# Kernel optimization log

Hardware: AMD Instinct MI355X
Metric: run time of the kernel (lower is better)

The kernel has to match this reference:

```python
import jax, jax.numpy as jnp
import numpy as np
import math

B, T, C, H = 2, 1024, 1024, 16
D = C // H


def setup_inputs() -> dict:
    key = jax.random.key(0)
    ks = jax.random.split(key, 7)
    scale = 1.0 / math.sqrt(C)
    q = jax.random.normal(ks[0], (B, T, C), dtype=jnp.float32)
    k = jax.random.normal(ks[1], (B, T, C), dtype=jnp.float32)
    v = jax.random.normal(ks[2], (B, T, C), dtype=jnp.float32)
    # causal mask, True = masked out (matches create_causal_mask)
    mask = jnp.triu(jnp.ones((T, T), dtype=bool), k=1)[None, None]
    Wk = jax.random.normal(ks[3], (C, C), dtype=jnp.float32) * scale
    bk = jax.random.normal(ks[4], (C,), dtype=jnp.float32) * scale
    Wc = jax.random.normal(ks[5], (C, C), dtype=jnp.float32) * scale
    bc = jax.random.normal(ks[6], (C,), dtype=jnp.float32) * scale
    return {"q": q, "k": k, "v": v, "mask": mask, "Wk": Wk, "bk": bk, "Wc": Wc, "bc": bc}


def reference(q, k, v, mask, Wk, bk, Wc, bc):
    # NOTE: original module uses self.k_attn for ALL of q, k, v (q_attn/v_attn unused).
    qB, qT, qC = q.shape
    kT = k.shape[1]
    qp = (q @ Wk.T + bk).reshape(qB, qT, H, D).transpose(0, 2, 1, 3)  # [B,H,Tq,D]
    kp = (k @ Wk.T + bk).reshape(qB, kT, H, D).transpose(0, 2, 1, 3)  # [B,H,Tk,D]
    vp = (v @ Wk.T + bk).reshape(qB, kT, H, D).transpose(0, 2, 1, 3)  # [B,H,Tk,D]
    att = jnp.einsum('bhqd,bhkd->bhqk', qp, kp) * (1.0 / math.sqrt(D))
    att = jnp.where(mask, -jnp.inf, att)
    att = jax.nn.softmax(att, axis=-1)
    y = jnp.einsum('bhqk,bhkd->bhqd', att, vp)
    y = y.transpose(0, 2, 1, 3).reshape(qB, qT, qC)
    return y @ Wc.T + bc
```

## Files before the change

### kernel.cpp

```cpp
#include <hip/hip_runtime.h>

#define T_DIM 1024
#define C_DIM 1024
#define H_DIM 16
#define D_DIM 64
#define KD    1024

typedef short  short8  __attribute__((ext_vector_type(8)));
typedef short  short4v __attribute__((ext_vector_type(4)));
typedef float  f32x4   __attribute__((ext_vector_type(4)));

__device__ __forceinline__ float bf2f(short s) {
  return __uint_as_float(((unsigned)(unsigned short)s) << 16);
}
__device__ __forceinline__ short f2bf(float f) {
  unsigned u = __float_as_uint(f);
  u += 0x7fffu + ((u >> 16) & 1u);
  return (short)(u >> 16);
}
__device__ __forceinline__ unsigned pk2(float lo, float hi) {
  return ((unsigned)(unsigned short)f2bf(lo)) | (((unsigned)(unsigned short)f2bf(hi)) << 16);
}

__device__ __forceinline__ void gl2lds16(const short* g, short* l) {
  __builtin_amdgcn_global_load_lds(
      (const __attribute__((address_space(1))) unsigned int*)(const void*)g,
      (__attribute__((address_space(3))) unsigned int*)(void*)l,
      16, 0, 0);
}

__device__ __forceinline__ short8 ldfrag(const void* p, size_t off, int isf32) {
  if (isf32) {
    const float* q = (const float*)p + off;
    f32x4 lo = *(const f32x4*)q;
    f32x4 hi = *(const f32x4*)(q + 4);
    short8 r;
#pragma unroll
    for (int j = 0; j < 4; ++j) { r[j] = f2bf(lo[j]); r[j + 4] = f2bf(hi[j]); }
    return r;
  }
  return *(const short8*)((const short*)p + off);
}
__device__ __forceinline__ float ldbias(const void* b, int i, int isf32) {
  return isf32 ? ((const float*)b)[i] : bf2f(((const short*)b)[i]);
}

__device__ __forceinline__ int detect_f32_inblock(const unsigned* w, int lane) {
  int c = 0;
#pragma unroll
  for (int i = 0; i < 4; ++i) {
    unsigned e = (w[lane * 4 + i] >> 7) & 0xffu;
    c += (e >= 110u && e <= 135u) ? 1 : 0;
  }
#pragma unroll
  for (int off = 32; off; off >>= 1) c += __shfl_xor(c, off);
  return (c < 128) ? 1 : 0;
}

#define SZE  ((size_t)2 * T_DIM * C_DIM)
#define QN   ((size_t)2097152)
#define WN   ((size_t)1048576)
#define BN   ((size_t)1024)
#define CVT_TOT (3 * QN + 2 * WN + 2 * BN)

__global__ __launch_bounds__(256) void cvt_k(const void* __restrict__ q,
                                             const void* __restrict__ k,
                                             const void* __restrict__ v,
                                             const void* __restrict__ wk,
                                             const void* __restrict__ wc,
                                             const void* __restrict__ bk,
                                             const void* __restrict__ bc,
                                             short* __restrict__ dst)
{
  const int lane = threadIdx.x & 63;
  const int f = detect_f32_inblock((const unsigned*)q, lane);

  const size_t idx = (size_t)blockIdx.x * 1024 + threadIdx.x * 4;
  if (idx >= CVT_TOT) return;
  const void* src;
  size_t loc;
  if      (idx <     QN)          { src = q;  loc = idx; }
  else if (idx < 2 * QN)          { src = k;  loc = idx - QN; }
  else if (idx < 3 * QN)          { src = v;  loc = idx - 2 * QN; }
  else if (idx < 3 * QN + WN)     { src = wk; loc = idx - 3 * QN; }
  else if (idx < 3 * QN + 2 * WN) { src = wc; loc = idx - 3 * QN - WN; }
  else if (idx < 3 * QN + 2 * WN + BN) { src = bk; loc = idx - 3 * QN - 2 * WN; }
  else                            { src = bc; loc = idx - 3 * QN - 2 * WN - BN; }

  short4v o;
  if (f) {
    f32x4 x = *(const f32x4*)((const float*)src + loc);
#pragma unroll
    for (int j = 0; j < 4; ++j) o[j] = f2bf(x[j]);
  } else {
    o = *(const short4v*)((const short*)src + loc);
  }
  *(short4v*)(dst + idx) = o;
}

__device__ __forceinline__ void stage8x8(const short* gsrc, short* S, int R0,
                                         int lane, int koff) {
  const int rw = R0 + (lane >> 3);
  const int q  = (lane & 7) ^ (rw & 7);
  gl2lds16(gsrc + (size_t)rw * KD + koff + q * 8, &S[R0 * 64]);
}
__device__ __forceinline__ short8 fragread64(const short* S, int row, int chunk) {
  const int sl = (row << 3) + (chunk ^ (row & 7));
  return *(const short8*)&S[sl << 3];
}

__global__ __launch_bounds__(256) void gemm_qkv_a(const short* __restrict__ X0,
                                                  const short* __restrict__ X1,
                                                  const short* __restrict__ X2,
                                                  const short* __restrict__ Wv,
                                                  const short* __restrict__ Bv,
                                                  short* __restrict__ outv)
{
  const int tid  = threadIdx.x;
  const int lane = tid & 63;
  const int wave = tid >> 6;
  const int col16 = lane & 15;
  const int quad  = lane >> 4;

  const int m0 = blockIdx.x * 128;
  const int c0 = blockIdx.y * 64;

  const int src = m0 >> 11;
  const short* Xv = (src == 0) ? X0 : (src == 1) ? X1 : X2;
  const int arow = m0 & 2047;
  const bool isv = (src == 2);
  short* outb = outv + (size_t)src * SZE;

  __shared__ short As[128 * 64];
  __shared__ short Bs[64 * 64];

  const short* Xg = Xv + (size_t)arow * KD;
  const short* Wg = Wv + (size_t)c0 * KD;

  f32x4 acc[2][4] = {};

  for (int k0 = 0; k0 < KD; k0 += 64) {
    if (k0) __syncthreads();
    stage8x8(Xg, As, wave * 32,      lane, k0);
    stage8x8(Xg, As, wave * 32 + 8,  lane, k0);
    stage8x8(Xg, As, wave * 32 + 16, lane, k0);
    stage8x8(Xg, As, wave * 32 + 24, lane, k0);
    stage8x8(Wg, Bs, wave * 16,      lane, k0);
    stage8x8(Wg, Bs, wave * 16 + 8,  lane, k0);
    __syncthreads();

#pragma unroll
    for (int kk = 0; kk < 2; ++kk) {
      short8 fx[2], fw[4];
#pragma unroll
      for (int i = 0; i < 2; ++i)
        fx[i] = fragread64(As, wave * 32 + i * 16 + col16, kk * 4 + quad);
#pragma unroll
      for (int j = 0; j < 4; ++j)
        fw[j] = fragread64(Bs, j * 16 + col16, kk * 4 + quad);

      if (isv) {
#pragma unroll
        for (int i = 0; i < 2; ++i)
#pragma unroll
          for (int j = 0; j < 4; ++j)
            acc[i][j] = __builtin_amdgcn_mfma_f32_16x16x32_bf16(fx[i], fw[j], acc[i][j], 0, 0, 0);
      } else {
#pragma unroll
        for (int i = 0; i < 2; ++i)
#pragma unroll
          for (int j = 0; j < 4; ++j)
            acc[i][j] = __builtin_amdgcn_mfma_f32_16x16x32_bf16(fw[j], fx[i], acc[i][j], 0, 0, 0);
      }
    }
  }

  if (isv) {
#pragma unroll
    for (int i = 0; i < 2; ++i) {
#pragma unroll
      for (int j = 0; j < 4; ++j) {
        const int c  = c0 + j * 16 + col16;
        const int t0 = arow + wave * 32 + i * 16 + quad * 4;
        const float bv = bf2f(Bv[c]);
        short4v pk;
#pragma unroll
        for (int r = 0; r < 4; ++r) pk[r] = f2bf(acc[i][j][r] + bv);
        const int bb = t0 >> 10, t = t0 & 1023, h = c >> 6, d = c & 63;
        size_t off = (size_t)((bb * H_DIM + h) * D_DIM + d) * T_DIM + t;
        *(short4v*)(outb + off) = pk;
      }
    }
  } else {
#pragma unroll
    for (int i = 0; i < 2; ++i) {
#pragma unroll
      for (int j = 0; j < 4; ++j) {
        const int m  = arow + wave * 32 + i * 16 + col16;
        const int cb = c0 + j * 16 + quad * 4;
        short4v bv4 = *(const short4v*)(Bv + cb);
        short4v pk;
#pragma unroll
        for (int r = 0; r < 4; ++r) pk[r] = f2bf(acc[i][j][r] + bf2f(bv4[r]));
        const int bb = m >> 10, t = m & 1023, h = cb >> 6, d = cb & 63;
        size_t off = ((size_t)(bb * H_DIM + h) << 16) + (size_t)t * D_DIM + d;
        *(short4v*)(outb + off) = pk;
      }
    }
  }
}

__global__ __launch_bounds__(256) void gemm_out_a(const short* __restrict__ Xb,
                                                  const short* __restrict__ Wv,
                                                  const short* __restrict__ Bv,
                                                  float* __restrict__ outv)
{
  const int tid  = threadIdx.x;
  const int lane = tid & 63;
  const int wave = tid >> 6;
  const int col16 = lane & 15;
  const int quad  = lane >> 4;
  const int wm = wave & 1;
  const int wn = wave >> 1;

  const int m0 = blockIdx.x * 64;
  const int c0 = blockIdx.y * 64;

  __shared__ short As[64 * 64];
  __shared__ short Bs[64 * 64];

  const short* Xg = Xb + (size_t)m0 * KD;
  const short* Wg = Wv + (size_t)c0 * KD;

  f32x4 acc[2][2] = {};

  for (int k0 = 0; k0 < KD; k0 += 64) {
    if (k0) __syncthreads();
    stage8x8(Xg, As, wave * 16,     lane, k0);
    stage8x8(Xg, As, wave * 16 + 8, lane, k0);
    stage8x8(Wg, Bs, wave * 16,     lane, k0);
    stage8x8(Wg, Bs, wave * 16 + 8, lane, k0);
    __syncthreads();

#pragma unroll
    for (int kk = 0; kk < 2; ++kk) {
      short8 fx[2], fw[2];
#pragma unroll
      for (int i = 0; i < 2; ++i)
        fx[i] = fragread64(As, wm * 32 + i * 16 + col16, kk * 4 + quad);
#pragma unroll
      for (int j = 0; j < 2; ++j)
        fw[j] = fragread64(Bs, wn * 32 + j * 16 + col16, kk * 4 + quad);

#pragma unroll
      for (int i = 0; i < 2; ++i)
#pragma unroll
        for (int j = 0; j < 2; ++j)
          acc[i][j] = __builtin_amdgcn_mfma_f32_16x16x32_bf16(fw[j], fx[i], acc[i][j], 0, 0, 0);
    }
  }

#pragma unroll
  for (int i = 0; i < 2; ++i) {
#pragma unroll
    for (int j = 0; j < 2; ++j) {
      const int m  = m0 + wm * 32 + i * 16 + col16;
      const int cb = c0 + wn * 32 + j * 16 + quad * 4;
      f32x4 pv;
#pragma unroll
      for (int r = 0; r < 4; ++r) pv[r] = acc[i][j][r] + bf2f(Bv[cb + r]);
      *(f32x4*)(outv + (size_t)m * C_DIM + cb) = pv;
    }
  }
}

#define LDSP 40

template<int KIND>
__global__ __launch_bounds__(256) void gemm2_k(const void* __restrict__ X0,
                                               const void* __restrict__ X1,
                                               const void* __restrict__ X2,
                                               const void* __restrict__ Wv,
                                               const void* __restrict__ Bv,
                                               void* __restrict__ outv)
{
  const int tid  = threadIdx.x;
  const int lane = tid & 63;
  const int wave = tid >> 6;
  const int col16 = lane & 15;
  const int quad  = lane >> 4;
  const int wm = wave & 1;
  const int wn = wave >> 1;

  const int f  = detect_f32_inblock((const unsigned*)Wv, lane);
  const int wf = f;
  const int xf = (KIND == 1) ? f : 0;

  const int m0 = blockIdx.x * 64;
  const int c0 = blockIdx.y * 64;

  const void* Xv = X0;
  int arow = m0;
  bool isv = false;
  short* outb = (short*)outv;
  if (KIND == 1) {
    const int src = m0 >> 11;
    Xv = (src == 0) ? X0 : (src == 1) ? X1 : X2;
    arow = m0 & 2047;
    isv = (src == 2);
    outb = (short*)outv + (size_t)src * SZE;
  }

  __shared__ short As[64 * LDSP];
  __shared__ short Bs[64 * LDSP];

  const int srow = tid >> 2;
  const int sc8  = tid & 3;

  f32x4 acc[2][2] = {};

  for (int k0 = 0; k0 < KD; k0 += 32) {
    short8 va = ldfrag(Xv, (size_t)(arow + srow) * KD + k0 + sc8 * 8, xf);
    short8 vb = ldfrag(Wv, (size_t)(c0 + srow) * KD + k0 + sc8 * 8, wf);
    if (k0) __syncthreads();
    *(short8*)&As[srow * LDSP + sc8 * 8] = va;
    *(short8*)&Bs[srow * LDSP + sc8 * 8] = vb;
    __syncthreads();

    short8 fx[2], fw[2];
#pragma unroll
    for (int i = 0; i < 2; ++i)
      fx[i] = *(const short8*)&As[(wm * 32 + i * 16 + col16) * LDSP + quad * 8];
#pragma unroll
    for (int j = 0; j < 2; ++j)
      fw[j] = *(const short8*)&Bs[(wn * 32 + j * 16 + col16) * LDSP + quad * 8];

    if (KIND == 1 && isv) {
#pragma unroll
      for (int i = 0; i < 2; ++i)
#pragma unroll
        for (int j = 0; j < 2; ++j)
          acc[i][j] = __builtin_amdgcn_mfma_f32_16x16x32_bf16(fx[i], fw[j], acc[i][j], 0, 0, 0);
    } else {
#pragma unroll
      for (int i = 0; i < 2; ++i)
#pragma unroll
        for (int j = 0; j < 2; ++j)
          acc[i][j] = __builtin_amdgcn_mfma_f32_16x16x32_bf16(fw[j], fx[i], acc[i][j], 0, 0, 0);
    }
  }

  if (KIND == 1 && isv) {
#pragma unroll
    for (int i = 0; i < 2; ++i) {
#pragma unroll
      for (int j = 0; j < 2; ++j) {
        const int c  = c0 + wn * 32 + j * 16 + col16;
        const int t0 = arow + wm * 32 + i * 16 + quad * 4;
        const float bv = ldbias(Bv, c, wf);
        short4v pk;
#pragma unroll
        for (int r = 0; r < 4; ++r) pk[r] = f2bf(acc[i][j][r] + bv);
        const int bb = t0 >> 10, t = t0 & 1023, h = c >> 6, d = c & 63;
        size_t off = (size_t)((bb * H_DIM + h) * D_DIM + d) * T_DIM + t;
        *(short4v*)(outb + off) = pk;
      }
    }
  } else {
#pragma unroll
    for (int i = 0; i < 2; ++i) {
#pragma unroll
      for (int j = 0; j < 2; ++j) {
        const int m  = arow + wm * 32 + i * 16 + col16;
        const int cb = c0 + wn * 32 + j * 16 + quad * 4;
        if (KIND == 0) {
          f32x4 pv;
#pragma unroll
          for (int r = 0; r < 4; ++r) pv[r] = acc[i][j][r] + ldbias(Bv, cb + r, wf);
          *(f32x4*)((float*)outv + (size_t)m * C_DIM + cb) = pv;
        } else {
          short4v pk;
#pragma unroll
          for (int r = 0; r < 4; ++r) pk[r] = f2bf(acc[i][j][r] + ldbias(Bv, cb + r, wf));
          const int bb = m >> 10, t = m & 1023, h = cb >> 6, d = cb & 63;
          size_t off = ((size_t)(bb * H_DIM + h) << 16) + (size_t)t * D_DIM + d;
          *(short4v*)(outb + off) = pk;
        }
      }
    }
  }
}

__global__ __launch_bounds__(256) void attn_k3(const short* __restrict__ qp,
                                               const short* __restrict__ kp,
                                               const short* __restrict__ vpt,
                                               short* __restrict__ y)
{
  const int lane = threadIdx.x & 63;
  const int wave = threadIdx.x >> 6;
  const int col  = lane & 15;
  const int quad = lane >> 4;
  const int bh = blockIdx.x;
  const int b = bh >> 4, h = bh & 15;
  const int qt = 63 - (int)blockIdx.y;
  const int q0 = qt * 16;
  const int myq = q0 + col;

  const short* qph = qp  + (size_t)bh * (T_DIM * D_DIM);
  const short* kph = kp  + (size_t)bh * (T_DIM * D_DIM);
  const short* vph = vpt + (size_t)bh * (D_DIM * T_DIM);

  const int nkt  = (q0 + 47) >> 5;
  const int base = nkt >> 2, rem = nkt & 3;
  const int cnt   = base + (wave < rem ? 1 : 0);
  const int start = wave * base + (wave < rem ? wave : rem);

  short8 bQ[2];
#pragma unroll
  for (int kk = 0; kk < 2; ++kk)
    bQ[kk] = *(const short8*)(qph + (size_t)(q0 + col) * D_DIM + kk * 32 + quad * 8);

  f32x4 O[4] = {};
  float rs = 0.0f;

  const int slA = col + ((quad & 1) * 32);
  const int slB = slA + 16;

#pragma unroll 2
  for (int kt = start; kt < start + cnt; ++kt) {
    const int kb = kt * 32;
    f32x4 st[2];
#pragma unroll
    for (int jt = 0; jt < 2; ++jt) {
      f32x4 s = {0.f, 0.f, 0.f, 0.f};
      const short* kbase = kph + (size_t)(kb + jt * 16 + col) * D_DIM + quad * 8;
      short8 aK0 = *(const short8*)(kbase);
      short8 aK1 = *(const short8*)(kbase + 32);
      __builtin_amdgcn_s_setprio(1);
      s = __builtin_amdgcn_mfma_f32_16x16x32_bf16(aK0, bQ[0], s, 0, 0, 0);
      s = __builtin_amdgcn_mfma_f32_16x16x32_bf16(aK1, bQ[1], s, 0, 0, 0);
      __builtin_amdgcn_s_setprio(0);
      st[jt] = s;
    }
#pragma unroll
    for (int jt = 0; jt < 2; ++jt) {
#pragma unroll
      for (int r = 0; r < 4; ++r) {
        const int key = kb + jt * 16 + quad * 4 + r;
        float p = __expf(st[jt][r] * 0.125f);
        p = (key > myq) ? 0.0f : p;
        st[jt][r] = p;
        rs += p;
      }
    }

    const int a0 = (int)pk2(st[0][0], st[0][1]);
    const int a1 = (int)pk2(st[0][2], st[0][3]);
    const int b0 = (int)pk2(st[1][0], st[1][1]);
    const int b1 = (int)pk2(st[1][2], st[1][3]);
    const int tA0 = __shfl(a0, slA, 64), tB0 = __shfl(b0, slA, 64);
    const int tA1 = __shfl(a1, slA, 64), tB1 = __shfl(b1, slA, 64);
    const int tA2 = __shfl(a0, slB, 64), tB2 = __shfl(b0, slB, 64);
    const int tA3 = __shfl(a1, slB, 64), tB3 = __shfl(b1, slB, 64);
    union { unsigned u[4]; short8 s8; } uu;
    uu.u[0] = (unsigned)((quad < 2) ? tA0 : tB0);
    uu.u[1] = (unsigned)((quad < 2) ? tA1 : tB1);
    uu.u[2] = (unsigned)((quad < 2) ? tA2 : tB2);
    uu.u[3] = (unsigned)((quad < 2) ? tA3 : tB3);
    const short8 bP32 = uu.s8;

    short8 aV[4];
#pragma unroll
    for (int dt = 0; dt < 4; ++dt)
      aV[dt] = *(const short8*)(vph + (size_t)(dt * 16 + col) * T_DIM + kb + quad * 8);
    __builtin_amdgcn_s_setprio(1);
#pragma unroll
    for (int dt = 0; dt < 4; ++dt)
      O[dt] = __builtin_amdgcn_mfma_f32_16x16x32_bf16(aV[dt], bP32, O[dt], 0, 0, 0);
    __builtin_amdgcn_s_setprio(0);
  }

  rs += __shfl_xor(rs, 16);
  rs += __shfl_xor(rs, 32);

  __shared__ float Om[4 * 4 * 16 * 16];
  __shared__ float Ll[4][16];

#pragma unroll
  for (int dt = 0; dt < 4; ++dt)
    *(f32x4*)&Om[(((wave * 4 + dt) * 16) + col) * 16 + quad * 4] = O[dt];
  if (quad == 0) Ll[wave][col] = rs;
  __syncthreads();

  float L = Ll[0][col] + Ll[1][col] + Ll[2][col] + Ll[3][col];
  f32x4 oacc = {0.f, 0.f, 0.f, 0.f};
#pragma unroll
  for (int w = 0; w < 4; ++w) {
    f32x4 ov = *(const f32x4*)&Om[(((w * 4 + wave) * 16) + col) * 16 + quad * 4];
#pragma unroll
    for (int r = 0; r < 4; ++r) oacc[r] += ov[r];
  }
  const float rl = 1.0f / L;
  const int t = q0 + col;
  const size_t ybase = ((size_t)(b * T_DIM + t)) * C_DIM + h * D_DIM + quad * 4;
  short4v pk;
#pragma unroll
  for (int r = 0; r < 4; ++r) pk[r] = f2bf(oacc[r] * rl);
  *(short4v*)(y + ybase + wave * 16) = pk;
}

extern "C" void kernel_launch(void* const* d_in, const int* in_sizes, int n_in,
                              void* d_out, int out_size, void* d_ws, size_t ws_size,
                              hipStream_t stream) {
  const void* q = d_in[0];
  const void* k = d_in[1];
  const void* v = d_in[2];
  int wi = (n_in >= 8 && in_sizes[4] == C_DIM * C_DIM) ? 4 : 3;
  const void* Wk = d_in[wi];
  const void* bk = d_in[wi + 1];
  const void* Wc = d_in[wi + 2];
  const void* bc = d_in[wi + 3];

  short* ws  = (short*)d_ws;
  short* qp  = ws;
  short* kp  = ws + SZE;
  short* vpt = ws + 2 * SZE;
  short* y   = ws + 3 * SZE;

  short* ext = ws + 4 * SZE;
  const size_t needed = (4 * SZE + CVT_TOT) * sizeof(short);
  const bool pre = (ws_size >= needed);

  dim3 blk(256);
  if (pre) {
    cvt_k<<<dim3((unsigned)((CVT_TOT + 1023) / 1024)), blk, 0, stream>>>(
        q, k, v, Wk, Wc, bk, bc, ext);
    const short* gq  = ext;
    const short* gk  = ext + QN;
    const short* gv  = ext + 2 * QN;
    const short* gwk = ext + 3 * QN;
    const short* gwc = ext + 3 * QN + WN;
    const short* gbk = ext + 3 * QN + 2 * WN;
    const short* gbc = ext + 3 * QN + 2 * WN + BN;

    gemm_qkv_a<<<dim3(48, 16), blk, 0, stream>>>(gq, gk, gv, gwk, gbk, qp);
    attn_k3<<<dim3(32, 64), blk, 0, stream>>>(qp, kp, vpt, y);
    gemm_out_a<<<dim3(32, 16), blk, 0, stream>>>(y, gwc, gbc, (float*)d_out);
  } else {
    gemm2_k<1><<<dim3(96, 16), blk, 0, stream>>>(q, k, v, Wk, bk, qp);
    attn_k3<<<dim3(32, 64), blk, 0, stream>>>(qp, kp, vpt, y);
    gemm2_k<0><<<dim3(32, 16), blk, 0, stream>>>(y, nullptr, nullptr, Wc, bc, d_out);
  }
}
```

Measured before the change: 159.7 us.

## Double-buffer LDS tiles in QKV and output projection GEMMs

Both projection GEMM kernels now use two LDS buffers. The next K-tile is staged while MFMAs run on the current one, which drops one barrier per iteration and overlaps global-to-LDS loads with compute. LDS use per block doubles, which may lower occupancy. How much overlap is gained depends on whether stage8x8 is an async direct-to-LDS load or a synchronous register copy.

```diff
diff --git a/kernel.cpp b/kernel.cpp
--- a/kernel.cpp
+++ b/kernel.cpp
@@ -131,33 +131,46 @@
   const bool isv = (src == 2);
   short* outb = outv + (size_t)src * SZE;
 
-  __shared__ short As[128 * 64];
-  __shared__ short Bs[64 * 64];
+  __shared__ short As[2][128 * 64];
+  __shared__ short Bs[2][64 * 64];
 
   const short* Xg = Xv + (size_t)arow * KD;
   const short* Wg = Wv + (size_t)c0 * KD;
 
   f32x4 acc[2][4] = {};
 
+  stage8x8(Xg, As[0], wave * 32,      lane, 0);
+  stage8x8(Xg, As[0], wave * 32 + 8,  lane, 0);
+  stage8x8(Xg, As[0], wave * 32 + 16, lane, 0);
+  stage8x8(Xg, As[0], wave * 32 + 24, lane, 0);
+  stage8x8(Wg, Bs[0], wave * 16,      lane, 0);
+  stage8x8(Wg, Bs[0], wave * 16 + 8,  lane, 0);
+  __syncthreads();
+
+  int cur = 0;
   for (int k0 = 0; k0 < KD; k0 += 64) {
-    if (k0) __syncthreads();
-    stage8x8(Xg, As, wave * 32,      lane, k0);
-    stage8x8(Xg, As, wave * 32 + 8,  lane, k0);
-    stage8x8(Xg, As, wave * 32 + 16, lane, k0);
-    stage8x8(Xg, As, wave * 32 + 24, lane, k0);
-    stage8x8(Wg, Bs, wave * 16,      lane, k0);
-    stage8x8(Wg, Bs, wave * 16 + 8,  lane, k0);
-    __syncthreads();
-
+    if (k0 + 64 < KD) {
+      short* An = As[cur ^ 1];
+      short* Bn = Bs[cur ^ 1];
+      stage8x8(Xg, An, wave * 32,      lane, k0 + 64);
+      stage8x8(Xg, An, wave * 32 + 8,  lane, k0 + 64);
+      stage8x8(Xg, An, wave * 32 + 16, lane, k0 + 64);
+      stage8x8(Xg, An, wave * 32 + 24, lane, k0 + 64);
+      stage8x8(Wg, Bn, wave * 16,      lane, k0 + 64);
+      stage8x8(Wg, Bn, wave * 16 + 8,  lane, k0 + 64);
+    }
+
+    const short* Ac = As[cur];
+    const short* Bc = Bs[cur];
 #pragma unroll
     for (int kk = 0; kk < 2; ++kk) {
       short8 fx[2], fw[4];
 #pragma unroll
       for (int i = 0; i < 2; ++i)
-        fx[i] = fragread64(As, wave * 32 + i * 16 + col16, kk * 4 + quad);
+        fx[i] = fragread64(Ac, wave * 32 + i * 16 + col16, kk * 4 + quad);
 #pragma unroll
       for (int j = 0; j < 4; ++j)
-        fw[j] = fragread64(Bs, j * 16 + col16, kk * 4 + quad);
+        fw[j] = fragread64(Bc, j * 16 + col16, kk * 4 + quad);
 
       if (isv) {
 #pragma unroll
@@ -173,6 +186,9 @@
             acc[i][j] = __builtin_amdgcn_mfma_f32_16x16x32_bf16(fw[j], fx[i], acc[i][j], 0, 0, 0);
       }
     }
+
+    __syncthreads();
+    cur ^= 1;
   }
 
   if (isv) {
@@ -226,31 +242,42 @@
   const int m0 = blockIdx.x * 64;
   const int c0 = blockIdx.y * 64;
 
-  __shared__ short As[64 * 64];
-  __shared__ short Bs[64 * 64];
+  __shared__ short As[2][64 * 64];
+  __shared__ short Bs[2][64 * 64];
 
   const short* Xg = Xb + (size_t)m0 * KD;
   const short* Wg = Wv + (size_t)c0 * KD;
 
   f32x4 acc[2][2] = {};
 
+  stage8x8(Xg, As[0], wave * 16,     lane, 0);
+  stage8x8(Xg, As[0], wave * 16 + 8, lane, 0);
+  stage8x8(Wg, Bs[0], wave * 16,     lane, 0);
+  stage8x8(Wg, Bs[0], wave * 16 + 8, lane, 0);
+  __syncthreads();
+
+  int cur = 0;
   for (int k0 = 0; k0 < KD; k0 += 64) {
-    if (k0) __syncthreads();
-    stage8x8(Xg, As, wave * 16,     lane, k0);
-    stage8x8(Xg, As, wave * 16 + 8, lane, k0);
-    stage8x8(Wg, Bs, wave * 16,     lane, k0);
-    stage8x8(Wg, Bs, wave * 16 + 8, lane, k0);
-    __syncthreads();
-
+    if (k0 + 64 < KD) {
+      short* An = As[cur ^ 1];
+      short* Bn = Bs[cur ^ 1];
+      stage8x8(Xg, An, wave * 16,     lane, k0 + 64);
+      stage8x8(Xg, An, wave * 16 + 8, lane, k0 + 64);
+      stage8x8(Wg, Bn, wave * 16,     lane, k0 + 64);
+      stage8x8(Wg, Bn, wave * 16 + 8, lane, k0 + 64);
+    }
+
+    const short* Ac = As[cur];
+    const short* Bc = Bs[cur];
 #pragma unroll
     for (int kk = 0; kk < 2; ++kk) {
       short8 fx[2], fw[2];
 #pragma unroll
       for (int i = 0; i < 2; ++i)
-        fx[i] = fragread64(As, wm * 32 + i * 16 + col16, kk * 4 + quad);
+        fx[i] = fragread64(Ac, wm * 32 + i * 16 + col16, kk * 4 + quad);
 #pragma unroll
       for (int j = 0; j < 2; ++j)
-        fw[j] = fragread64(Bs, wn * 32 + j * 16 + col16, kk * 4 + quad);
+        fw[j] = fragread64(Bc, wn * 32 + j * 16 + col16, kk * 4 + quad);
 
 #pragma unroll
       for (int i = 0; i < 2; ++i)
@@ -258,6 +285,9 @@
         for (int j = 0; j < 2; ++j)
           acc[i][j] = __builtin_amdgcn_mfma_f32_16x16x32_bf16(fw[j], fx[i], acc[i][j], 0, 0, 0);
     }
+
+    __syncthreads();
+    cur ^= 1;
   }
 
 #pragma unroll
```

New measurement: 160.6 us. About the same (+0.5%).
